# Kernel tuning notes

Hardware: AMD Instinct MI355X
Metric: run time of the kernel (lower is better)

Reference implementation:

```python
import jax, jax.numpy as jnp
import numpy as np
import math

B, S, D, H = 2, 2048, 1024, 16
DK = D // H


def setup_inputs() -> dict:
    key = jax.random.key(0)
    k1, k2, k3, k4, k5, k6 = jax.random.split(key, 6)
    scale = 1.0 / math.sqrt(D)
    return {
        "query": jax.random.normal(k1, (B, S, D), dtype=jnp.float32),
        "key": jax.random.normal(k2, (B, S, D), dtype=jnp.float32),
        "value": jax.random.normal(k3, (B, S, D), dtype=jnp.float32),
        "Wqkv": jax.random.normal(k4, (D, D), dtype=jnp.float32) * scale,
        "Wout": jax.random.normal(k5, (D, D), dtype=jnp.float32) * scale,
        "mask": jax.random.randint(k6, (B, 1, S, S), 0, 2, dtype=jnp.int32),
    }


def reference(query, key, value, Wqkv, Wout, mask):
    # Single shared QKV projection (same weight applied to q, k, v), no bias.
    q = query @ Wqkv.T
    k = key @ Wqkv.T
    v = value @ Wqkv.T
    # Faithful to the original: reshape (B, S, D) -> (B, H, S, DK) directly
    # (torch .reshape(n_batches, h, -1, d_k), NOT view+transpose).
    q = q.reshape(B, H, S, DK)
    k = k.reshape(B, H, S, DK)
    v = v.reshape(B, H, S, DK)
    scores = jnp.einsum("bhqd,bhkd->bhqk", q, k) / math.sqrt(DK)
    scores = jnp.where(mask == 0, jnp.float32(-1e9), scores)
    p_attn = jax.nn.softmax(scores, axis=-1)  # dropout is identity in eval
    x = jnp.einsum("bhqk,bhkd->bhqd", p_attn, v)  # [B,H,S,DK]
    x = x.transpose(0, 2, 1, 3).reshape(B, S, H * DK)
    return x @ Wout.T
```

## Files before the change

### kernel.cpp

```cpp
#include <hip/hip_runtime.h>
#include <stdint.h>


typedef __bf16 bf16;
typedef __bf16 bf16x8 __attribute__((ext_vector_type(8)));
typedef __bf16 bf16x4 __attribute__((ext_vector_type(4)));
typedef float f32x4 __attribute__((ext_vector_type(4)));

#define MFMA16(a, b, c) __builtin_amdgcn_mfma_f32_16x16x32_bf16((a), (b), (c), 0, 0, 0)
#define EXP2(x) __builtin_amdgcn_exp2f(x)

static constexpr int BATCH = 2;
static constexpr int SEQ = 2048;
static constexpr int DIM = 1024;
static constexpr int DK = 64;
static constexpr float QSCALE = 0.125f * 1.44269504088896340736f;

__device__ inline void gload16(const void* g, void* l) {
  __builtin_amdgcn_global_load_lds((const __attribute__((address_space(1))) void*)g,
                                   (__attribute__((address_space(3))) void*)l, 16, 0, 0);
}

__global__ __launch_bounds__(256) void prep_kernel(
    const int* __restrict__ mask, unsigned long long* __restrict__ bits,
    const float* __restrict__ sq, const float* __restrict__ sk, const float* __restrict__ sv,
    const float* __restrict__ swq, const float* __restrict__ swo,
    bf16* __restrict__ dq, bf16* __restrict__ dk, bf16* __restrict__ dv,
    bf16* __restrict__ dwq, bf16* __restrict__ dwo) {
  const int bid = blockIdx.x;
  const int tid = threadIdx.x;
  if (bid < 8192) {
    const int lane = tid & 63, wv = tid >> 6;
    const int ebase = (bid * 4 + wv) * 256;
    unsigned long long w[4];
#pragma unroll
    for (int j = 0; j < 4; ++j) {
      int m = mask[ebase + j * 64 + lane];
      w[j] = __ballot(m != 0);
    }
    if (lane == 0) {
#pragma unroll
      for (int j = 0; j < 4; ++j) bits[(ebase >> 6) + j] = w[j];
    }
    return;
  }
  int r = bid - 8192;
  const float* s;
  bf16* d;
  int i;
  if (r < 6144) {
    s = (r < 2048) ? sq : (r < 4096) ? sk : sv;
    d = (r < 2048) ? dq : (r < 4096) ? dk : dv;
    i = (r & 2047) * 256 + tid;
  } else {
    r -= 6144;
    s = (r < 512) ? swq : swo;
    d = (r < 512) ? dwq : dwo;
    i = (r & 511) * 256 + tid;
  }
  const float4 a = ((const float4*)s)[2 * i];
  const float4 b = ((const float4*)s)[2 * i + 1];
  bf16x8 v;
  v[0] = (bf16)a.x;
  v[1] = (bf16)a.y;
  v[2] = (bf16)a.z;
  v[3] = (bf16)a.w;
  v[4] = (bf16)b.x;
  v[5] = (bf16)b.y;
  v[6] = (bf16)b.z;
  v[7] = (bf16)b.w;
  ((bf16x8*)d)[i] = v;
}

template <int BM, int BN, int NBX, int NBY, int NBZ, typename TC>
__global__ __launch_bounds__(256, 2) void gemm_bt_lds(
    const bf16* __restrict__ A0, const bf16* __restrict__ A1, const bf16* __restrict__ A2,
    const bf16* __restrict__ W, TC* __restrict__ C0, TC* __restrict__ C1, TC* __restrict__ C2,
    float scale0) {
  constexpr int K = 1024, N = 1024;
  constexpr int MT = BM / 32, NT = BN / 32;
  constexpr int SA = BM / 64, SB = BN / 64;
  constexpr int NB = NBX * NBY * NBZ;
  __shared__ __align__(16) bf16 As[2][BM * 32];
  __shared__ __align__(16) bf16 Bs[2][BN * 32];

  const int lin = blockIdx.x + NBX * (blockIdx.y + NBY * blockIdx.z);
  const int l = (lin & 7) * (NB / 8) + (lin >> 3);
  const int lx = l % NBX;
  const int ly = (l / NBX) % NBY;
  const int lz = l / (NBX * NBY);

  const bf16* A = (lz == 0) ? A0 : (lz == 1) ? A1 : A2;
  TC* C = (lz == 0) ? C0 : (lz == 1) ? C1 : C2;
  const float sc = (lz == 0) ? scale0 : 1.0f;

  const int tid = threadIdx.x;
  const int lane = tid & 63;
  const int wv = tid >> 6;
  const int wm = wv >> 1, wn = wv & 1;
  const int lrow = lane & 15, quad = lane >> 4;
  const int m0 = ly * BM, n0 = lx * BN;

  const int r0 = tid >> 2, c0 = (tid & 3) * 8;
  const bf16* pa[SA];
  const bf16* pb[SB];
#pragma unroll
  for (int s = 0; s < SA; ++s) pa[s] = A + (size_t)(m0 + s * 64 + r0) * K + c0;
#pragma unroll
  for (int s = 0; s < SB; ++s) pb[s] = W + (size_t)(n0 + s * 64 + r0) * K + c0;

  const f32x4 fz = {0.f, 0.f, 0.f, 0.f};
  f32x4 acc[MT][NT];
#pragma unroll
  for (int i = 0; i < MT; ++i)
#pragma unroll
    for (int j = 0; j < NT; ++j) acc[i][j] = fz;

#pragma unroll
  for (int s = 0; s < SA; ++s) gload16(pa[s], &As[0][s * 2048 + tid * 8]);
#pragma unroll
  for (int s = 0; s < SB; ++s) gload16(pb[s], &Bs[0][s * 2048 + tid * 8]);
  __syncthreads();

  for (int t = 0; t < K / 32; ++t) {
    const int cur = t & 1;
    if (t + 1 < K / 32) {
      const int k1 = (t + 1) * 32;
#pragma unroll
      for (int s = 0; s < SA; ++s) gload16(pa[s] + k1, &As[cur ^ 1][s * 2048 + tid * 8]);
#pragma unroll
      for (int s = 0; s < SB; ++s) gload16(pb[s] + k1, &Bs[cur ^ 1][s * 2048 + tid * 8]);
    }
    bf16x8 af[MT], bfr[NT];
#pragma unroll
    for (int mt = 0; mt < MT; ++mt)
      af[mt] = *(const bf16x8*)(&As[cur][(wm * (BM / 2) + mt * 16 + lrow) * 32 + quad * 8]);
#pragma unroll
    for (int nt = 0; nt < NT; ++nt)
      bfr[nt] = *(const bf16x8*)(&Bs[cur][(wn * (BN / 2) + nt * 16 + lrow) * 32 + quad * 8]);
#pragma unroll
    for (int mt = 0; mt < MT; ++mt)
#pragma unroll
      for (int nt = 0; nt < NT; ++nt) acc[mt][nt] = MFMA16(af[mt], bfr[nt], acc[mt][nt]);
    __syncthreads();
  }

#pragma unroll
  for (int mt = 0; mt < MT; ++mt) {
    const int gm = m0 + wm * (BM / 2) + mt * 16 + quad * 4;
#pragma unroll
    for (int nt = 0; nt < NT; ++nt) {
      const int gn = n0 + wn * (BN / 2) + nt * 16 + lrow;
#pragma unroll
      for (int r = 0; r < 4; ++r) C[(size_t)(gm + r) * N + gn] = (TC)(acc[mt][nt][r] * sc);
    }
  }
}

__global__ __launch_bounds__(256, 2) void attn_kernel(const bf16* __restrict__ Qg,
                                                      const bf16* __restrict__ Kg,
                                                      const bf16* __restrict__ Vg,
                                                      const unsigned* __restrict__ bits,
                                                      bf16* __restrict__ Y) {
  constexpr int LQ = 72;
  __shared__ bf16 Qs[128 * LQ];
  __shared__ bf16 Ks[64 * LQ];
  __shared__ bf16 Vts[64 * LQ];
  __shared__ bf16 Ps[4][32 * LQ];

  const int tid = threadIdx.x;
  const int lane = tid & 63;
  const int wv = tid >> 6;
  const int lrow = lane & 15, quad = lane >> 4;
  const int bh = blockIdx.y;
  const int b = bh >> 4, h = bh & 15;
  const int q0 = blockIdx.x * 128;

  const bf16* Qh = Qg + (size_t)bh * (SEQ * DK);
  const bf16* Kh = Kg + (size_t)bh * (SEQ * DK);
  const bf16* Vh = Vg + (size_t)bh * (SEQ * DK);

#pragma unroll
  for (int i = 0; i < 4; ++i) {
    int s = tid + i * 256;
    int row = s >> 3, c8 = (s & 7) * 8;
    *(uint4*)(&Qs[row * LQ + c8]) = *(const uint4*)(Qh + (size_t)(q0 + row) * DK + c8);
  }

  const int krow = tid >> 3;
  const int kc8 = (tid & 7) * 8;
  const bf16* pk0 = Kh + (size_t)krow * DK + kc8;
  const bf16* pk1 = Kh + (size_t)(krow + 32) * DK + kc8;
  const int vn2 = tid & 31;
  const int vk2b = tid >> 5;
  const bf16* pv0 = Vh + (size_t)(vk2b + 0) * 2 * DK + vn2 * 2;
  const bf16* pv1 = Vh + (size_t)(vk2b + 8) * 2 * DK + vn2 * 2;
  const bf16* pv2 = Vh + (size_t)(vk2b + 16) * 2 * DK + vn2 * 2;
  const bf16* pv3 = Vh + (size_t)(vk2b + 24) * 2 * DK + vn2 * 2;

  uint4 kr0, kr1;
  uint32_t va[4], vb[4];

  kr0 = *(const uint4*)(pk0);
  kr1 = *(const uint4*)(pk1);
  va[0] = *(const uint32_t*)(pv0);
  vb[0] = *(const uint32_t*)(pv0 + DK);
  va[1] = *(const uint32_t*)(pv1);
  vb[1] = *(const uint32_t*)(pv1 + DK);
  va[2] = *(const uint32_t*)(pv2);
  vb[2] = *(const uint32_t*)(pv2 + DK);
  va[3] = *(const uint32_t*)(pv3);
  vb[3] = *(const uint32_t*)(pv3 + DK);
  *(uint4*)(&Ks[krow * LQ + kc8]) = kr0;
  *(uint4*)(&Ks[(krow + 32) * LQ + kc8]) = kr1;
#pragma unroll
  for (int i = 0; i < 4; ++i) {
    uint32_t t0 = (va[i] & 0xffffu) | (vb[i] << 16);
    uint32_t t1 = (va[i] >> 16) | (vb[i] & 0xffff0000u);
    *(uint32_t*)(&Vts[(vn2 * 2) * LQ + (vk2b + i * 8) * 2]) = t0;
    *(uint32_t*)(&Vts[(vn2 * 2 + 1) * LQ + (vk2b + i * 8) * 2]) = t1;
  }
  __syncthreads();

  bf16x8 qf[2][2];
#pragma unroll
  for (int nt = 0; nt < 2; ++nt)
#pragma unroll
    for (int ks = 0; ks < 2; ++ks)
      qf[nt][ks] = *(const bf16x8*)(&Qs[(wv * 32 + nt * 16 + lrow) * LQ + ks * 32 + quad * 8]);
  __syncthreads();

  const f32x4 fz = {0.f, 0.f, 0.f, 0.f};
  f32x4 of_t[4][2];
#pragma unroll
  for (int i = 0; i < 4; ++i)
#pragma unroll
    for (int j = 0; j < 2; ++j) of_t[i][j] = fz;
  float lsum[2] = {0.f, 0.f};

  const unsigned* bitrow = bits + (size_t)b * SEQ * (SEQ / 32);

  for (int kt = 0; kt < 32; ++kt) {
    const int cur = kt & 1;
    bf16* kb = cur ? Qs : Ks;
    bf16* vbuf = cur ? (Qs + 64 * LQ) : Vts;
    if (kt + 1 < 32) {
      const size_t adv = (size_t)(kt + 1) * 64 * DK;
      kr0 = *(const uint4*)(pk0 + adv);
      kr1 = *(const uint4*)(pk1 + adv);
      va[0] = *(const uint32_t*)(pv0 + adv);
      vb[0] = *(const uint32_t*)(pv0 + adv + DK);
      va[1] = *(const uint32_t*)(pv1 + adv);
      vb[1] = *(const uint32_t*)(pv1 + adv + DK);
      va[2] = *(const uint32_t*)(pv2 + adv);
      vb[2] = *(const uint32_t*)(pv2 + adv + DK);
      va[3] = *(const uint32_t*)(pv3 + adv);
      vb[3] = *(const uint32_t*)(pv3 + adv + DK);
    }
    uint2 mwn[2];
#pragma unroll
    for (int nt = 0; nt < 2; ++nt) {
      int row = q0 + wv * 32 + nt * 16 + lrow;
      mwn[nt] = *(const uint2*)(bitrow + (size_t)row * (SEQ / 32) + kt * 2);
    }

    f32x4 st[4][2];
#pragma unroll
    for (int mt = 0; mt < 4; ++mt)
#pragma unroll
      for (int nt = 0; nt < 2; ++nt) st[mt][nt] = fz;
#pragma unroll
    for (int ks = 0; ks < 2; ++ks) {
#pragma unroll
      for (int mt = 0; mt < 4; ++mt) {
        bf16x8 kfv = *(const bf16x8*)(kb + (mt * 16 + lrow) * LQ + ks * 32 + quad * 8);
#pragma unroll
        for (int nt = 0; nt < 2; ++nt) st[mt][nt] = MFMA16(kfv, qf[nt][ks], st[mt][nt]);
      }
    }

#pragma unroll
    for (int nt = 0; nt < 2; ++nt) {
      uint32_t ux = mwn[nt].x >> (quad * 4);
      uint32_t uy = mwn[nt].y >> (quad * 4);
      float psum = 0.f;
#pragma unroll
      for (int mt = 0; mt < 4; ++mt) {
        uint32_t u = (mt & 2) ? uy : ux;
        int sh = (mt & 1) << 4;
        bf16x4 pk;
#pragma unroll
        for (int r = 0; r < 4; ++r) {
          float p = EXP2(st[mt][nt][r]);
          p = ((u >> (sh + r)) & 1u) ? p : 0.f;
          psum += p;
          pk[r] = (bf16)p;
        }
        *(bf16x4*)(&Ps[wv][(nt * 16 + lrow) * LQ + mt * 16 + quad * 4]) = pk;
      }
      lsum[nt] += psum;
    }

#pragma unroll
    for (int ks = 0; ks < 2; ++ks) {
      bf16x8 avf[4], bpf[2];
#pragma unroll
      for (int dkt = 0; dkt < 4; ++dkt)
        avf[dkt] = *(const bf16x8*)(vbuf + (dkt * 16 + lrow) * LQ + ks * 32 + quad * 8);
#pragma unroll
      for (int rt = 0; rt < 2; ++rt)
        bpf[rt] = *(const bf16x8*)(&Ps[wv][(rt * 16 + lrow) * LQ + ks * 32 + quad * 8]);
#pragma unroll
      for (int dkt = 0; dkt < 4; ++dkt)
#pragma unroll
        for (int rt = 0; rt < 2; ++rt) of_t[dkt][rt] = MFMA16(avf[dkt], bpf[rt], of_t[dkt][rt]);
    }

    if (kt + 1 < 32) {
      bf16* kbn = cur ? Ks : Qs;
      bf16* vbn = cur ? Vts : (Qs + 64 * LQ);
      *(uint4*)(kbn + krow * LQ + kc8) = kr0;
      *(uint4*)(kbn + (krow + 32) * LQ + kc8) = kr1;
#pragma unroll
      for (int i = 0; i < 4; ++i) {
        uint32_t t0 = (va[i] & 0xffffu) | (vb[i] << 16);
        uint32_t t1 = (va[i] >> 16) | (vb[i] & 0xffff0000u);
        *(uint32_t*)(vbn + (vn2 * 2) * LQ + (vk2b + i * 8) * 2) = t0;
        *(uint32_t*)(vbn + (vn2 * 2 + 1) * LQ + (vk2b + i * 8) * 2) = t1;
      }
    }
    __syncthreads();
  }

  float linv[2];
#pragma unroll
  for (int nt = 0; nt < 2; ++nt) {
    float v = lsum[nt];
    v += __shfl_xor(v, 16);
    v += __shfl_xor(v, 32);
    linv[nt] = 1.0f / fmaxf(v, 1e-20f);
  }

#pragma unroll
  for (int dkt = 0; dkt < 4; ++dkt)
#pragma unroll
    for (int rt = 0; rt < 2; ++rt) {
      bf16x4 o;
#pragma unroll
      for (int j = 0; j < 4; ++j) o[j] = (bf16)(of_t[dkt][rt][j] * linv[rt]);
      const int row = q0 + wv * 32 + rt * 16 + lrow;
      *(bf16x4*)(&Y[((size_t)b * SEQ + row) * DIM + h * 64 + dkt * 16 + quad * 4]) = o;
    }
}

extern "C" void kernel_launch(void* const* d_in, const int* in_sizes, int n_in,
                              void* d_out, int out_size, void* d_ws, size_t ws_size,
                              hipStream_t stream) {
  const float* query = (const float*)d_in[0];
  const float* key = (const float*)d_in[1];
  const float* value = (const float*)d_in[2];
  const float* Wqkv = (const float*)d_in[3];
  const float* Wout = (const float*)d_in[4];
  const int* mask = (const int*)d_in[5];
  float* out = (float*)d_out;

  char* ws = (char*)d_ws;
  bf16* qin = (bf16*)(ws);
  bf16* kin = (bf16*)(ws + 8388608);
  bf16* vin = (bf16*)(ws + 16777216);
  bf16* Wq = (bf16*)(ws + 25165824);
  bf16* Wo = (bf16*)(ws + 27262976);
  bf16* q = (bf16*)(ws + 29360128);
  bf16* k = (bf16*)(ws + 37748736);
  bf16* v = (bf16*)(ws + 46137344);
  bf16* y = (bf16*)(ws);
  unsigned long long* bits64 = (unsigned long long*)(ws + 54525952);

  prep_kernel<<<15360, 256, 0, stream>>>(mask, bits64, query, key, value, Wqkv, Wout,
                                         qin, kin, vin, Wq, Wo);

  gemm_bt_lds<128, 256, 4, 32, 3, bf16>
      <<<dim3(4, 32, 3), 256, 0, stream>>>(qin, kin, vin, Wq, q, k, v, QSCALE);

  attn_kernel<<<dim3(16, 32), 256, 0, stream>>>(q, k, v, (const unsigned*)bits64, y);

  gemm_bt_lds<64, 128, 8, 64, 1, float>
      <<<dim3(8, 64, 1), 256, 0, stream>>>(y, y, y, Wo, out, out, out, 1.0f);
}
```

Before: 255.8 us.

## Fuse fp32-to-bf16 activation conversion into QKV projection GEMM loads

```diff
diff --git a/kernel.cpp b/kernel.cpp
--- a/kernel.cpp
+++ b/kernel.cpp
@@ -21,45 +21,9 @@
                                    (__attribute__((address_space(3))) void*)l, 16, 0, 0);
 }
 
-__global__ __launch_bounds__(256) void prep_kernel(
-    const int* __restrict__ mask, unsigned long long* __restrict__ bits,
-    const float* __restrict__ sq, const float* __restrict__ sk, const float* __restrict__ sv,
-    const float* __restrict__ swq, const float* __restrict__ swo,
-    bf16* __restrict__ dq, bf16* __restrict__ dk, bf16* __restrict__ dv,
-    bf16* __restrict__ dwq, bf16* __restrict__ dwo) {
-  const int bid = blockIdx.x;
-  const int tid = threadIdx.x;
-  if (bid < 8192) {
-    const int lane = tid & 63, wv = tid >> 6;
-    const int ebase = (bid * 4 + wv) * 256;
-    unsigned long long w[4];
-#pragma unroll
-    for (int j = 0; j < 4; ++j) {
-      int m = mask[ebase + j * 64 + lane];
-      w[j] = __ballot(m != 0);
-    }
-    if (lane == 0) {
-#pragma unroll
-      for (int j = 0; j < 4; ++j) bits[(ebase >> 6) + j] = w[j];
-    }
-    return;
-  }
-  int r = bid - 8192;
-  const float* s;
-  bf16* d;
-  int i;
-  if (r < 6144) {
-    s = (r < 2048) ? sq : (r < 4096) ? sk : sv;
-    d = (r < 2048) ? dq : (r < 4096) ? dk : dv;
-    i = (r & 2047) * 256 + tid;
-  } else {
-    r -= 6144;
-    s = (r < 512) ? swq : swo;
-    d = (r < 512) ? dwq : dwo;
-    i = (r & 511) * 256 + tid;
-  }
-  const float4 a = ((const float4*)s)[2 * i];
-  const float4 b = ((const float4*)s)[2 * i + 1];
+__device__ inline bf16x8 cvt8(const float* p) {
+  const float4 a = *(const float4*)p;
+  const float4 b = *(const float4*)(p + 4);
   bf16x8 v;
   v[0] = (bf16)a.x;
   v[1] = (bf16)a.y;
@@ -69,19 +33,51 @@
   v[5] = (bf16)b.y;
   v[6] = (bf16)b.z;
   v[7] = (bf16)b.w;
-  ((bf16x8*)d)[i] = v;
-}
-
-template <int BM, int BN, int NBX, int NBY, int NBZ, typename TC>
-__global__ __launch_bounds__(256, 2) void gemm_bt_lds(
-    const bf16* __restrict__ A0, const bf16* __restrict__ A1, const bf16* __restrict__ A2,
+  return v;
+}
+
+__global__ __launch_bounds__(256) void prep_kernel(const int* __restrict__ mask,
+                                                   unsigned long long* __restrict__ bits,
+                                                   const float* __restrict__ swq,
+                                                   const float* __restrict__ swo,
+                                                   bf16* __restrict__ dwq,
+                                                   bf16* __restrict__ dwo) {
+  const int bid = blockIdx.x;
+  const int tid = threadIdx.x;
+  if (bid < 8192) {
+    const int lane = tid & 63, wv = tid >> 6;
+    const int ebase = (bid * 4 + wv) * 256;
+    unsigned long long w[4];
+#pragma unroll
+    for (int j = 0; j < 4; ++j) {
+      int m = mask[ebase + j * 64 + lane];
+      w[j] = __ballot(m != 0);
+    }
+    if (lane == 0) {
+#pragma unroll
+      for (int j = 0; j < 4; ++j) bits[(ebase >> 6) + j] = w[j];
+    }
+    return;
+  }
+  int r = bid - 8192;
+  const float* s = (r < 512) ? swq : swo;
+  bf16* d = (r < 512) ? dwq : dwo;
+  const int i = (r & 511) * 256 + tid;
+  ((bf16x8*)d)[i] = cvt8(&s[8 * i]);
+}
+
+template <int BM, int BN, int NBX, int NBY, int NBZ, int MINW, typename TA, typename TC>
+__global__ __launch_bounds__(256, MINW) void gemm_bt_lds(
+    const TA* __restrict__ A0, const TA* __restrict__ A1, const TA* __restrict__ A2,
     const bf16* __restrict__ W, TC* __restrict__ C0, TC* __restrict__ C1, TC* __restrict__ C2,
     float scale0) {
   constexpr int K = 1024, N = 1024;
   constexpr int MT = BM / 32, NT = BN / 32;
-  constexpr int SA = BM / 64, SB = BN / 64;
+  constexpr bool AF32 = sizeof(TA) == 4;
+  constexpr int PA = AF32 ? (BM / 32) : (BM / 64);
+  constexpr int PB = BN / 64;
   constexpr int NB = NBX * NBY * NBZ;
-  __shared__ __align__(16) bf16 As[2][BM * 32];
+  __shared__ __align__(16) TA As[2][BM * 32];
   __shared__ __align__(16) bf16 Bs[2][BN * 32];
 
   const int lin = blockIdx.x + NBX * (blockIdx.y + NBY * blockIdx.z);
@@ -90,7 +86,7 @@
   const int ly = (l / NBX) % NBY;
   const int lz = l / (NBX * NBY);
 
-  const bf16* A = (lz == 0) ? A0 : (lz == 1) ? A1 : A2;
+  const TA* A = (lz == 0) ? A0 : (lz == 1) ? A1 : A2;
   TC* C = (lz == 0) ? C0 : (lz == 1) ? C1 : C2;
   const float sc = (lz == 0) ? scale0 : 1.0f;
 
@@ -101,13 +97,18 @@
   const int lrow = lane & 15, quad = lane >> 4;
   const int m0 = ly * BM, n0 = lx * BN;
 
-  const int r0 = tid >> 2, c0 = (tid & 3) * 8;
-  const bf16* pa[SA];
-  const bf16* pb[SB];
-#pragma unroll
-  for (int s = 0; s < SA; ++s) pa[s] = A + (size_t)(m0 + s * 64 + r0) * K + c0;
-#pragma unroll
-  for (int s = 0; s < SB; ++s) pb[s] = W + (size_t)(n0 + s * 64 + r0) * K + c0;
+  const int rA = AF32 ? (tid >> 3) : (tid >> 2);
+  const int cA = AF32 ? ((tid & 7) * 4) : ((tid & 3) * 8);
+  constexpr int ROWSA = AF32 ? 32 : 64;
+  constexpr int ELEMA = AF32 ? 1024 : 2048;
+  constexpr int EPTA = AF32 ? 4 : 8;
+  const int rB = tid >> 2, cB = (tid & 3) * 8;
+  const TA* pa[PA];
+  const bf16* pb[PB];
+#pragma unroll
+  for (int p = 0; p < PA; ++p) pa[p] = A + (size_t)(m0 + p * ROWSA + rA) * K + cA;
+#pragma unroll
+  for (int p = 0; p < PB; ++p) pb[p] = W + (size_t)(n0 + p * 64 + rB) * K + cB;
 
   const f32x4 fz = {0.f, 0.f, 0.f, 0.f};
   f32x4 acc[MT][NT];
@@ -117,9 +118,9 @@
     for (int j = 0; j < NT; ++j) acc[i][j] = fz;
 
 #pragma unroll
-  for (int s = 0; s < SA; ++s) gload16(pa[s], &As[0][s * 2048 + tid * 8]);
-#pragma unroll
-  for (int s = 0; s < SB; ++s) gload16(pb[s], &Bs[0][s * 2048 + tid * 8]);
+  for (int p = 0; p < PA; ++p) gload16(pa[p], &As[0][p * ELEMA + tid * EPTA]);
+#pragma unroll
+  for (int p = 0; p < PB; ++p) gload16(pb[p], &Bs[0][p * 2048 + tid * 8]);
   __syncthreads();
 
   for (int t = 0; t < K / 32; ++t) {
@@ -127,14 +128,20 @@
     if (t + 1 < K / 32) {
       const int k1 = (t + 1) * 32;
 #pragma unroll
-      for (int s = 0; s < SA; ++s) gload16(pa[s] + k1, &As[cur ^ 1][s * 2048 + tid * 8]);
-#pragma unroll
-      for (int s = 0; s < SB; ++s) gload16(pb[s] + k1, &Bs[cur ^ 1][s * 2048 + tid * 8]);
+      for (int p = 0; p < PA; ++p) gload16(pa[p] + k1, &As[cur ^ 1][p * ELEMA + tid * EPTA]);
+#pragma unroll
+      for (int p = 0; p < PB; ++p) gload16(pb[p] + k1, &Bs[cur ^ 1][p * 2048 + tid * 8]);
     }
     bf16x8 af[MT], bfr[NT];
 #pragma unroll
-    for (int mt = 0; mt < MT; ++mt)
-      af[mt] = *(const bf16x8*)(&As[cur][(wm * (BM / 2) + mt * 16 + lrow) * 32 + quad * 8]);
+    for (int mt = 0; mt < MT; ++mt) {
+      const int row = wm * (BM / 2) + mt * 16 + lrow;
+      if constexpr (AF32) {
+        af[mt] = cvt8((const float*)&As[cur][row * 32 + quad * 8]);
+      } else {
+        af[mt] = *(const bf16x8*)(&As[cur][row * 32 + quad * 8]);
+      }
+    }
 #pragma unroll
     for (int nt = 0; nt < NT; ++nt)
       bfr[nt] = *(const bf16x8*)(&Bs[cur][(wn * (BN / 2) + nt * 16 + lrow) * 32 + quad * 8]);
@@ -365,25 +372,21 @@
   float* out = (float*)d_out;
 
   char* ws = (char*)d_ws;
-  bf16* qin = (bf16*)(ws);
-  bf16* kin = (bf16*)(ws + 8388608);
-  bf16* vin = (bf16*)(ws + 16777216);
-  bf16* Wq = (bf16*)(ws + 25165824);
-  bf16* Wo = (bf16*)(ws + 27262976);
-  bf16* q = (bf16*)(ws + 29360128);
-  bf16* k = (bf16*)(ws + 37748736);
-  bf16* v = (bf16*)(ws + 46137344);
-  bf16* y = (bf16*)(ws);
-  unsigned long long* bits64 = (unsigned long long*)(ws + 54525952);
-
-  prep_kernel<<<15360, 256, 0, stream>>>(mask, bits64, query, key, value, Wqkv, Wout,
-                                         qin, kin, vin, Wq, Wo);
-
-  gemm_bt_lds<128, 256, 4, 32, 3, bf16>
-      <<<dim3(4, 32, 3), 256, 0, stream>>>(qin, kin, vin, Wq, q, k, v, QSCALE);
+  bf16* Wq = (bf16*)(ws);
+  bf16* Wo = (bf16*)(ws + 2097152);
+  bf16* q = (bf16*)(ws + 4194304);
+  bf16* k = (bf16*)(ws + 12582912);
+  bf16* v = (bf16*)(ws + 20971520);
+  bf16* y = (bf16*)(ws + 29360128);
+  unsigned long long* bits64 = (unsigned long long*)(ws + 37748736);
+
+  prep_kernel<<<9216, 256, 0, stream>>>(mask, bits64, Wqkv, Wout, Wq, Wo);
+
+  gemm_bt_lds<128, 128, 8, 32, 3, 3, float, bf16>
+      <<<dim3(8, 32, 3), 256, 0, stream>>>(query, key, value, Wq, q, k, v, QSCALE);
 
   attn_kernel<<<dim3(16, 32), 256, 0, stream>>>(q, k, v, (const unsigned*)bits64, y);
 
-  gemm_bt_lds<64, 128, 8, 64, 1, float>
+  gemm_bt_lds<64, 128, 8, 64, 1, 2, bf16, float>
       <<<dim3(8, 64, 1), 256, 0, stream>>>(y, y, y, Wo, out, out, out, 1.0f);
 }
```

New measurement: 340.0 us. +32.9%, slower.

## Shrink attention query tile to 64 rows and retile QKV GEMM

Applied to the files above, without the earlier changes.

```diff
diff --git a/kernel.cpp b/kernel.cpp
--- a/kernel.cpp
+++ b/kernel.cpp
@@ -72,14 +72,14 @@
   ((bf16x8*)d)[i] = v;
 }
 
-template <int BM, int BN, int NBX, int NBY, int NBZ, typename TC>
-__global__ __launch_bounds__(256, 2) void gemm_bt_lds(
+template <int BM, int BN, int NBX, int NBY, int NBZ, int MINW, typename TC>
+__global__ __launch_bounds__(256, MINW) void gemm_bt_lds(
     const bf16* __restrict__ A0, const bf16* __restrict__ A1, const bf16* __restrict__ A2,
     const bf16* __restrict__ W, TC* __restrict__ C0, TC* __restrict__ C1, TC* __restrict__ C2,
     float scale0) {
   constexpr int K = 1024, N = 1024;
   constexpr int MT = BM / 32, NT = BN / 32;
-  constexpr int SA = BM / 64, SB = BN / 64;
+  constexpr int PA = BM / 64, PB = BN / 64;
   constexpr int NB = NBX * NBY * NBZ;
   __shared__ __align__(16) bf16 As[2][BM * 32];
   __shared__ __align__(16) bf16 Bs[2][BN * 32];
@@ -102,12 +102,12 @@
   const int m0 = ly * BM, n0 = lx * BN;
 
   const int r0 = tid >> 2, c0 = (tid & 3) * 8;
-  const bf16* pa[SA];
-  const bf16* pb[SB];
-#pragma unroll
-  for (int s = 0; s < SA; ++s) pa[s] = A + (size_t)(m0 + s * 64 + r0) * K + c0;
-#pragma unroll
-  for (int s = 0; s < SB; ++s) pb[s] = W + (size_t)(n0 + s * 64 + r0) * K + c0;
+  const bf16* pa[PA];
+  const bf16* pb[PB];
+#pragma unroll
+  for (int p = 0; p < PA; ++p) pa[p] = A + (size_t)(m0 + p * 64 + r0) * K + c0;
+#pragma unroll
+  for (int p = 0; p < PB; ++p) pb[p] = W + (size_t)(n0 + p * 64 + r0) * K + c0;
 
   const f32x4 fz = {0.f, 0.f, 0.f, 0.f};
   f32x4 acc[MT][NT];
@@ -117,9 +117,9 @@
     for (int j = 0; j < NT; ++j) acc[i][j] = fz;
 
 #pragma unroll
-  for (int s = 0; s < SA; ++s) gload16(pa[s], &As[0][s * 2048 + tid * 8]);
-#pragma unroll
-  for (int s = 0; s < SB; ++s) gload16(pb[s], &Bs[0][s * 2048 + tid * 8]);
+  for (int p = 0; p < PA; ++p) gload16(pa[p], &As[0][p * 2048 + tid * 8]);
+#pragma unroll
+  for (int p = 0; p < PB; ++p) gload16(pb[p], &Bs[0][p * 2048 + tid * 8]);
   __syncthreads();
 
   for (int t = 0; t < K / 32; ++t) {
@@ -127,9 +127,9 @@
     if (t + 1 < K / 32) {
       const int k1 = (t + 1) * 32;
 #pragma unroll
-      for (int s = 0; s < SA; ++s) gload16(pa[s] + k1, &As[cur ^ 1][s * 2048 + tid * 8]);
-#pragma unroll
-      for (int s = 0; s < SB; ++s) gload16(pb[s] + k1, &Bs[cur ^ 1][s * 2048 + tid * 8]);
+      for (int p = 0; p < PA; ++p) gload16(pa[p] + k1, &As[cur ^ 1][p * 2048 + tid * 8]);
+#pragma unroll
+      for (int p = 0; p < PB; ++p) gload16(pb[p] + k1, &Bs[cur ^ 1][p * 2048 + tid * 8]);
     }
     bf16x8 af[MT], bfr[NT];
 #pragma unroll
@@ -157,16 +157,15 @@
   }
 }
 
-__global__ __launch_bounds__(256, 2) void attn_kernel(const bf16* __restrict__ Qg,
+__global__ __launch_bounds__(256, 4) void attn_kernel(const bf16* __restrict__ Qg,
                                                       const bf16* __restrict__ Kg,
                                                       const bf16* __restrict__ Vg,
                                                       const unsigned* __restrict__ bits,
                                                       bf16* __restrict__ Y) {
   constexpr int LQ = 72;
-  __shared__ bf16 Qs[128 * LQ];
   __shared__ bf16 Ks[64 * LQ];
   __shared__ bf16 Vts[64 * LQ];
-  __shared__ bf16 Ps[4][32 * LQ];
+  __shared__ bf16 Ps[4][16 * LQ];
 
   const int tid = threadIdx.x;
   const int lane = tid & 63;
@@ -174,18 +173,17 @@
   const int lrow = lane & 15, quad = lane >> 4;
   const int bh = blockIdx.y;
   const int b = bh >> 4, h = bh & 15;
-  const int q0 = blockIdx.x * 128;
+  const int q0 = blockIdx.x * 64;
+  const int qrow = q0 + wv * 16 + lrow;
 
   const bf16* Qh = Qg + (size_t)bh * (SEQ * DK);
   const bf16* Kh = Kg + (size_t)bh * (SEQ * DK);
   const bf16* Vh = Vg + (size_t)bh * (SEQ * DK);
 
-#pragma unroll
-  for (int i = 0; i < 4; ++i) {
-    int s = tid + i * 256;
-    int row = s >> 3, c8 = (s & 7) * 8;
-    *(uint4*)(&Qs[row * LQ + c8]) = *(const uint4*)(Qh + (size_t)(q0 + row) * DK + c8);
-  }
+  bf16x8 qf[2];
+#pragma unroll
+  for (int ks = 0; ks < 2; ++ks)
+    qf[ks] = *(const bf16x8*)(Qh + (size_t)qrow * DK + ks * 32 + quad * 8);
 
   const int krow = tid >> 3;
   const int kc8 = (tid & 7) * 8;
@@ -222,28 +220,15 @@
   }
   __syncthreads();
 
-  bf16x8 qf[2][2];
-#pragma unroll
-  for (int nt = 0; nt < 2; ++nt)
-#pragma unroll
-    for (int ks = 0; ks < 2; ++ks)
-      qf[nt][ks] = *(const bf16x8*)(&Qs[(wv * 32 + nt * 16 + lrow) * LQ + ks * 32 + quad * 8]);
-  __syncthreads();
-
   const f32x4 fz = {0.f, 0.f, 0.f, 0.f};
-  f32x4 of_t[4][2];
-#pragma unroll
-  for (int i = 0; i < 4; ++i)
-#pragma unroll
-    for (int j = 0; j < 2; ++j) of_t[i][j] = fz;
-  float lsum[2] = {0.f, 0.f};
+  f32x4 of_t[4];
+#pragma unroll
+  for (int i = 0; i < 4; ++i) of_t[i] = fz;
+  float lsum = 0.f;
 
   const unsigned* bitrow = bits + (size_t)b * SEQ * (SEQ / 32);
 
   for (int kt = 0; kt < 32; ++kt) {
-    const int cur = kt & 1;
-    bf16* kb = cur ? Qs : Ks;
-    bf16* vbuf = cur ? (Qs + 64 * LQ) : Vts;
     if (kt + 1 < 32) {
       const size_t adv = (size_t)(kt + 1) * 64 * DK;
       kr0 = *(const uint4*)(pk0 + adv);
@@ -257,32 +242,23 @@
       va[3] = *(const uint32_t*)(pv3 + adv);
       vb[3] = *(const uint32_t*)(pv3 + adv + DK);
     }
-    uint2 mwn[2];
-#pragma unroll
-    for (int nt = 0; nt < 2; ++nt) {
-      int row = q0 + wv * 32 + nt * 16 + lrow;
-      mwn[nt] = *(const uint2*)(bitrow + (size_t)row * (SEQ / 32) + kt * 2);
-    }
-
-    f32x4 st[4][2];
-#pragma unroll
-    for (int mt = 0; mt < 4; ++mt)
-#pragma unroll
-      for (int nt = 0; nt < 2; ++nt) st[mt][nt] = fz;
+    const uint2 mwn = *(const uint2*)(bitrow + (size_t)qrow * (SEQ / 32) + kt * 2);
+
+    f32x4 st[4];
+#pragma unroll
+    for (int mt = 0; mt < 4; ++mt) st[mt] = fz;
 #pragma unroll
     for (int ks = 0; ks < 2; ++ks) {
 #pragma unroll
       for (int mt = 0; mt < 4; ++mt) {
-        bf16x8 kfv = *(const bf16x8*)(kb + (mt * 16 + lrow) * LQ + ks * 32 + quad * 8);
-#pragma unroll
-        for (int nt = 0; nt < 2; ++nt) st[mt][nt] = MFMA16(kfv, qf[nt][ks], st[mt][nt]);
+        bf16x8 kfv = *(const bf16x8*)(&Ks[(mt * 16 + lrow) * LQ + ks * 32 + quad * 8]);
+        st[mt] = MFMA16(kfv, qf[ks], st[mt]);
       }
     }
 
-#pragma unroll
-    for (int nt = 0; nt < 2; ++nt) {
-      uint32_t ux = mwn[nt].x >> (quad * 4);
-      uint32_t uy = mwn[nt].y >> (quad * 4);
+    {
+      uint32_t ux = mwn.x >> (quad * 4);
+      uint32_t uy = mwn.y >> (quad * 4);
       float psum = 0.f;
 #pragma unroll
       for (int mt = 0; mt < 4; ++mt) {
@@ -291,66 +267,53 @@
         bf16x4 pk;
 #pragma unroll
         for (int r = 0; r < 4; ++r) {
-          float p = EXP2(st[mt][nt][r]);
+          float p = EXP2(st[mt][r]);
           p = ((u >> (sh + r)) & 1u) ? p : 0.f;
           psum += p;
           pk[r] = (bf16)p;
         }
-        *(bf16x4*)(&Ps[wv][(nt * 16 + lrow) * LQ + mt * 16 + quad * 4]) = pk;
+        *(bf16x4*)(&Ps[wv][lrow * LQ + mt * 16 + quad * 4]) = pk;
       }
-      lsum[nt] += psum;
+      lsum += psum;
     }
 
 #pragma unroll
     for (int ks = 0; ks < 2; ++ks) {
-      bf16x8 avf[4], bpf[2];
-#pragma unroll
-      for (int dkt = 0; dkt < 4; ++dkt)
-        avf[dkt] = *(const bf16x8*)(vbuf + (dkt * 16 + lrow) * LQ + ks * 32 + quad * 8);
-#pragma unroll
-      for (int rt = 0; rt < 2; ++rt)
-        bpf[rt] = *(const bf16x8*)(&Ps[wv][(rt * 16 + lrow) * LQ + ks * 32 + quad * 8]);
-#pragma unroll
-      for (int dkt = 0; dkt < 4; ++dkt)
-#pragma unroll
-        for (int rt = 0; rt < 2; ++rt) of_t[dkt][rt] = MFMA16(avf[dkt], bpf[rt], of_t[dkt][rt]);
-    }
-
+      bf16x8 bpf = *(const bf16x8*)(&Ps[wv][lrow * LQ + ks * 32 + quad * 8]);
+#pragma unroll
+      for (int dkt = 0; dkt < 4; ++dkt) {
+        bf16x8 avf = *(const bf16x8*)(&Vts[(dkt * 16 + lrow) * LQ + ks * 32 + quad * 8]);
+        of_t[dkt] = MFMA16(avf, bpf, of_t[dkt]);
+      }
+    }
+
+    __syncthreads();
     if (kt + 1 < 32) {
-      bf16* kbn = cur ? Ks : Qs;
-      bf16* vbn = cur ? Vts : (Qs + 64 * LQ);
-      *(uint4*)(kbn + krow * LQ + kc8) = kr0;
-      *(uint4*)(kbn + (krow + 32) * LQ + kc8) = kr1;
+      *(uint4*)(&Ks[krow * LQ + kc8]) = kr0;
+      *(uint4*)(&Ks[(krow + 32) * LQ + kc8]) = kr1;
 #pragma unroll
       for (int i = 0; i < 4; ++i) {
         uint32_t t0 = (va[i] & 0xffffu) | (vb[i] << 16);
         uint32_t t1 = (va[i] >> 16) | (vb[i] & 0xffff0000u);
-        *(uint32_t*)(vbn + (vn2 * 2) * LQ + (vk2b + i * 8) * 2) = t0;
-        *(uint32_t*)(vbn + (vn2 * 2 + 1) * LQ + (vk2b + i * 8) * 2) = t1;
+        *(uint32_t*)(&Vts[(vn2 * 2) * LQ + (vk2b + i * 8) * 2]) = t0;
+        *(uint32_t*)(&Vts[(vn2 * 2 + 1) * LQ + (vk2b + i * 8) * 2]) = t1;
       }
-    }
-    __syncthreads();
-  }
-
-  float linv[2];
-#pragma unroll
-  for (int nt = 0; nt < 2; ++nt) {
-    float v = lsum[nt];
-    v += __shfl_xor(v, 16);
-    v += __shfl_xor(v, 32);
-    linv[nt] = 1.0f / fmaxf(v, 1e-20f);
-  }
-
-#pragma unroll
-  for (int dkt = 0; dkt < 4; ++dkt)
-#pragma unroll
-    for (int rt = 0; rt < 2; ++rt) {
-      bf16x4 o;
-#pragma unroll
-      for (int j = 0; j < 4; ++j) o[j] = (bf16)(of_t[dkt][rt][j] * linv[rt]);
-      const int row = q0 + wv * 32 + rt * 16 + lrow;
-      *(bf16x4*)(&Y[((size_t)b * SEQ + row) * DIM + h * 64 + dkt * 16 + quad * 4]) = o;
-    }
+      __syncthreads();
+    }
+  }
+
+  float v = lsum;
+  v += __shfl_xor(v, 16);
+  v += __shfl_xor(v, 32);
+  const float linv = 1.0f / fmaxf(v, 1e-20f);
+
+#pragma unroll
+  for (int dkt = 0; dkt < 4; ++dkt) {
+    bf16x4 o;
+#pragma unroll
+    for (int j = 0; j < 4; ++j) o[j] = (bf16)(of_t[dkt][j] * linv);
+    *(bf16x4*)(&Y[((size_t)b * SEQ + qrow) * DIM + h * 64 + dkt * 16 + quad * 4]) = o;
+  }
 }
 
 extern "C" void kernel_launch(void* const* d_in, const int* in_sizes, int n_in,
@@ -379,11 +342,11 @@
   prep_kernel<<<15360, 256, 0, stream>>>(mask, bits64, query, key, value, Wqkv, Wout,
                                          qin, kin, vin, Wq, Wo);
 
-  gemm_bt_lds<128, 256, 4, 32, 3, bf16>
-      <<<dim3(4, 32, 3), 256, 0, stream>>>(qin, kin, vin, Wq, q, k, v, QSCALE);
-
-  attn_kernel<<<dim3(16, 32), 256, 0, stream>>>(q, k, v, (const unsigned*)bits64, y);
-
-  gemm_bt_lds<64, 128, 8, 64, 1, float>
+  gemm_bt_lds<128, 128, 8, 32, 3, 3, bf16>
+      <<<dim3(8, 32, 3), 256, 0, stream>>>(qin, kin, vin, Wq, q, k, v, QSCALE);
+
+  attn_kernel<<<dim3(32, 32), 256, 0, stream>>>(q, k, v, (const unsigned*)bits64, y);
+
+  gemm_bt_lds<64, 128, 8, 64, 1, 2, float>
       <<<dim3(8, 64, 1), 256, 0, stream>>>(y, y, y, Wo, out, out, out, 1.0f);
 }
```

Result: no change. 260.7 us (+1.9%).
